# Kernel tuning notes

Hardware: AMD Instinct MI355X
Metric: run time of the kernel (lower is better)

## Reference

```python
import jax, jax.numpy as jnp
import numpy as np

BOUNDS = 1.3
RES = 512
N_COMP = 16
N_LAMB = 3        # n_lamb_params[0]
VEC_PARAM = 3     # vecSize_params[0]
OUT_DIM = 32
N_PTS = 2097152

MAT_X = np.array([0, 0, 1])  # matMode first coord per plane
MAT_Y = np.array([1, 2, 2])  # matMode second coord per plane
VEC_M = np.array([2, 1, 0])  # vecMode


def _sample2d(grid, x, y):
    # grid: [C,H,W]; x,y: [N] in [-1,1]; bilinear, align_corners=True
    C, H, W = grid.shape
    ix = (x + 1.0) * 0.5 * (W - 1)
    iy = (y + 1.0) * 0.5 * (H - 1)
    x0 = jnp.floor(ix)
    y0 = jnp.floor(iy)
    wx = ix - x0
    wy = iy - y0
    x0i = jnp.clip(x0.astype(jnp.int32), 0, W - 1)
    x1i = jnp.clip(x0i + 1, 0, W - 1)
    y0i = jnp.clip(y0.astype(jnp.int32), 0, H - 1)
    y1i = jnp.clip(y0i + 1, 0, H - 1)
    g = lambda yi, xi: grid[:, yi, xi]  # [C,N]
    return (g(y0i, x0i) * (1 - wy) * (1 - wx) + g(y0i, x1i) * (1 - wy) * wx
            + g(y1i, x0i) * wy * (1 - wx) + g(y1i, x1i) * wy * wx)


def _sample1d(vec, y):
    # vec: [C,L]; y: [N] in [-1,1]; linear interp along L (grid width is 1,
    # x coord is always 0 in the torch code so it reduces to 1D)
    C, L = vec.shape
    iy = (y + 1.0) * 0.5 * (L - 1)
    y0 = jnp.floor(iy)
    wy = iy - y0
    y0i = jnp.clip(y0.astype(jnp.int32), 0, L - 1)
    y1i = jnpp_clip = jnp.clip(y0i + 1, 0, L - 1)
    return vec[:, y0i] * (1 - wy) + vec[:, y1i] * wy


def setup_inputs() -> dict:
    key = jax.random.key(0)
    k1, k2, k3, k4, k5 = jax.random.split(key, 5)
    pts = (jax.random.uniform(k1, (N_PTS, 3), jnp.float32) * 2.0 - 1.0) * BOUNDS
    timestamps = jax.random.uniform(k2, (N_PTS, 1), jnp.float32) * 2.0 - 1.0
    scale = 0.1
    planes = scale * jax.random.normal(k3, (3, N_COMP, RES, RES), jnp.float32)
    lines = scale * jax.random.normal(k4, (3, N_COMP, RES), jnp.float32)
    params_grid = scale * jnp.ones((N_LAMB, VEC_PARAM), jnp.float32)
    # torch Linear(19 -> 32, bias=False): weight [out, in]
    W = jax.random.normal(k5, (OUT_DIM, N_COMP + N_LAMB), jnp.float32) * (1.0 / np.sqrt(N_COMP + N_LAMB))
    return {"pts": pts, "timestamps": timestamps, "planes": planes,
            "lines": lines, "params_grid": params_grid, "W": W}


def reference(pts, timestamps, planes, lines, params_grid, W):
    # normalize_aabb with aabb = [[b,b,b],[-b,-b,-b]]
    pts_n = (pts - BOUNDS) * (2.0 / (-2.0 * BOUNDS)) - 1.0  # -> [-1,1]
    # torch code detaches sampling coordinates
    pts_n = jax.lax.stop_gradient(pts_n)
    t = jax.lax.stop_gradient(timestamps[:, 0])
    plane_x = pts_n[:, MAT_X].T  # [3,N]
    plane_y = pts_n[:, MAT_Y].T  # [3,N]
    line_c = pts_n[:, VEC_M].T   # [3,N]
    plane_feat = jax.vmap(_sample2d)(planes, plane_x, plane_y)  # [3,C,N]
    line_feat = jax.vmap(_sample1d)(lines, line_c)              # [3,C,N]
    coef = jnp.sum(plane_feat * line_feat, axis=0)              # [C,N]
    pfeat = _sample1d(params_grid, t)                           # [3,N]
    feats = jnp.concatenate([coef, pfeat], axis=0).T            # [N,19]
    return feats @ W.T                                          # [N,32]
```

## Files before the change

kernel.cpp:

```cpp
#include <hip/hip_runtime.h>
#include <hip/hip_bf16.h>

#define RES 512
#define NC 16
#define NPLANES 3

typedef float f32x4 __attribute__((ext_vector_type(4)));

static __device__ inline float nt_loadf(const float* p) { return __builtin_nontemporal_load(p); }
static __device__ inline void nt_store4(float* p, f32x4 v) {
  __builtin_nontemporal_store(v, (f32x4*)p);
}
static __device__ inline float bf_lo(unsigned u) { return __uint_as_float(u << 16); }
static __device__ inline float bf_hi(unsigned u) { return __uint_as_float(u & 0xFFFF0000u); }

__global__ __launch_bounds__(256) void transpose_planes_k(
    const float* __restrict__ in, __hip_bfloat16* __restrict__ out)
{
  __shared__ float sm[NC][64 + 1];
  int b   = blockIdx.x;
  int xb  = b & 7;
  int y   = (b >> 3) & 511;
  int p   = b >> 12;
  int x0  = xb << 6;
  int tid = threadIdx.x;
#pragma unroll
  for (int k = 0; k < 4; ++k) {
    int e = tid + k * 256;
    int c = e >> 6, x = e & 63;
    sm[c][x] = nt_loadf(&in[(size_t)((p * NC + c) * RES + y) * RES + x0 + x]);
  }
  __syncthreads();
#pragma unroll
  for (int k = 0; k < 4; ++k) {
    int e = tid + k * 256;
    int x = e >> 4, c = e & 15;
    out[(size_t)((p * RES + y) * RES + x0 + x) * NC + c] = __float2bfloat16(sm[c][x]);
  }
}

__global__ void transpose_lines_k(const float* __restrict__ in, float* __restrict__ out)
{
  int i = blockIdx.x * 256 + threadIdx.x;
  if (i >= NPLANES * RES * NC) return;
  int c = i & 15;
  int l = (i >> 4) & 511;
  int p = i >> 13;
  out[i] = nt_loadf(&in[(p * NC + c) * RES + l]);
}

template <bool TP>
__global__ __launch_bounds__(256) void visnerf_main_k(
    const float* __restrict__ pts, const float* __restrict__ ts,
    const __hip_bfloat16* __restrict__ planesb, const float* __restrict__ lines,
    const float* __restrict__ planes_f32, const float* __restrict__ lines_f32,
    const float* __restrict__ pg, const float* __restrict__ W,
    float* __restrict__ out, int N)
{
  __shared__ __align__(16) float sW[32 * 20];
  __shared__ __align__(16) float st[256 * 32];
  __shared__ float spg[9];
  int tid = threadIdx.x;
  for (int e = tid; e < 640; e += 256) {
    int o = e / 20, c = e - o * 20;
    sW[e] = (c < 19) ? W[o * 19 + c] : 0.0f;
  }
  if (tid < 9) spg[tid] = pg[tid];
  __syncthreads();

  int i  = blockIdx.x * 256 + tid;
  int ii = (i < N) ? i : (N - 1);
  float px = nt_loadf(&pts[ii * 3 + 0]);
  float py = nt_loadf(&pts[ii * 3 + 1]);
  float pz = nt_loadf(&pts[ii * 3 + 2]);
  float t  = nt_loadf(&ts[ii]);

  const float kk = (float)(2.0 / (-2.0 * 1.3));
  float nn[3];
  nn[0] = (px - 1.3f) * kk - 1.0f;
  nn[1] = (py - 1.3f) * kk - 1.0f;
  nn[2] = (pz - 1.3f) * kk - 1.0f;

  float feats[20];
#pragma unroll
  for (int c = 0; c < 20; ++c) feats[c] = 0.0f;

  const int matx[3] = {0, 0, 1};
  const int maty[3] = {1, 2, 2};
  const int vecm[3] = {2, 1, 0};

#pragma unroll
  for (int q = 0; q < 3; ++q) {
    float x  = nn[matx[q]], y = nn[maty[q]], lc = nn[vecm[q]];
    float ix = (x + 1.0f) * 0.5f * (float)(RES - 1);
    float iy = (y + 1.0f) * 0.5f * (float)(RES - 1);
    float fx = floorf(ix), fy = floorf(iy);
    float wx = ix - fx, wy = iy - fy;
    int x0 = (int)fx; x0 = x0 < 0 ? 0 : (x0 > RES - 1 ? RES - 1 : x0);
    int y0 = (int)fy; y0 = y0 < 0 ? 0 : (y0 > RES - 1 ? RES - 1 : y0);
    int x1 = (x0 + 1 > RES - 1) ? RES - 1 : x0 + 1;
    int y1 = (y0 + 1 > RES - 1) ? RES - 1 : y0 + 1;

    float il = (lc + 1.0f) * 0.5f * (float)(RES - 1);
    float fl = floorf(il);
    float wl = il - fl;
    int l0 = (int)fl; l0 = l0 < 0 ? 0 : (l0 > RES - 1 ? RES - 1 : l0);
    int l1 = (l0 + 1 > RES - 1) ? RES - 1 : l0 + 1;

    float w00 = (1.0f - wy) * (1.0f - wx);
    float w01 = (1.0f - wy) * wx;
    float w10 = wy * (1.0f - wx);
    float w11 = wy * wx;
    float wl0 = 1.0f - wl;

    if (TP) {
      const uint4* ta = (const uint4*)(planesb + (size_t)((q * RES + y0) * RES + x0) * NC);
      const uint4* tb = (const uint4*)(planesb + (size_t)((q * RES + y0) * RES + x1) * NC);
      const uint4* tc = (const uint4*)(planesb + (size_t)((q * RES + y1) * RES + x0) * NC);
      const uint4* td = (const uint4*)(planesb + (size_t)((q * RES + y1) * RES + x1) * NC);
      const float4* L0 = (const float4*)(lines + (size_t)(q * RES + l0) * NC);
      const float4* L1 = (const float4*)(lines + (size_t)(q * RES + l1) * NC);
#pragma unroll
      for (int h = 0; h < 2; ++h) {
        uint4 ua = ta[h], ub = tb[h], uc = tc[h], ud = td[h];
        float4 e0a = L0[2 * h + 0], e0b = L0[2 * h + 1];
        float4 e1a = L1[2 * h + 0], e1b = L1[2 * h + 1];
        const unsigned* pa = &ua.x;
        const unsigned* pb = &ub.x;
        const unsigned* pc = &uc.x;
        const unsigned* pd = &ud.x;
        const float* q0 = &e0a.x;
        const float* q1 = &e1a.x;
#pragma unroll
        for (int w = 0; w < 4; ++w) {
          int c0 = h * 8 + 2 * w;
          float pf0 = w00 * bf_lo(pa[w]) + w01 * bf_lo(pb[w]) +
                      w10 * bf_lo(pc[w]) + w11 * bf_lo(pd[w]);
          float pf1 = w00 * bf_hi(pa[w]) + w01 * bf_hi(pb[w]) +
                      w10 * bf_hi(pc[w]) + w11 * bf_hi(pd[w]);
          float lf0 = (w < 2) ? (wl0 * q0[2 * w] + wl * q1[2 * w])
                              : (wl0 * (&e0b.x)[2 * w - 4] + wl * (&e1b.x)[2 * w - 4]);
          float lf1 = (w < 2) ? (wl0 * q0[2 * w + 1] + wl * q1[2 * w + 1])
                              : (wl0 * (&e0b.x)[2 * w - 3] + wl * (&e1b.x)[2 * w - 3]);
          feats[c0 + 0] += pf0 * lf0;
          feats[c0 + 1] += pf1 * lf1;
        }
      }
    } else {
#pragma unroll 4
      for (int c = 0; c < NC; ++c) {
        const float* pl = planes_f32 + (size_t)(q * NC + c) * RES * RES;
        float a  = pl[y0 * RES + x0], b = pl[y0 * RES + x1];
        float c2 = pl[y1 * RES + x0], d = pl[y1 * RES + x1];
        const float* ln = lines_f32 + (size_t)(q * NC + c) * RES;
        float lf = ln[l0] * wl0 + ln[l1] * wl;
        feats[c] += (w00 * a + w01 * b + w10 * c2 + w11 * d) * lf;
      }
    }
  }

  {
    float it = (t + 1.0f) * 0.5f * 2.0f;
    float ft = floorf(it);
    float wt = it - ft;
    int t0 = (int)ft; t0 = t0 < 0 ? 0 : (t0 > 2 ? 2 : t0);
    int t1 = (t0 + 1 > 2) ? 2 : t0 + 1;
    feats[16] = spg[0 + t0] * (1.0f - wt) + spg[0 + t1] * wt;
    feats[17] = spg[3 + t0] * (1.0f - wt) + spg[3 + t1] * wt;
    feats[18] = spg[6 + t0] * (1.0f - wt) + spg[6 + t1] * wt;
    feats[19] = 0.0f;
  }

  float res[32];
#pragma unroll
  for (int o = 0; o < 32; ++o) {
    const float4* wr = (const float4*)(sW + o * 20);
    float acc = 0.0f;
#pragma unroll
    for (int k = 0; k < 5; ++k) {
      float4 wv = wr[k];
      acc += feats[4 * k + 0] * wv.x + feats[4 * k + 1] * wv.y +
             feats[4 * k + 2] * wv.z + feats[4 * k + 3] * wv.w;
    }
    res[o] = acc;
  }

#pragma unroll
  for (int o = 0; o < 32; ++o)
    st[tid * 32 + ((o + tid) & 31)] = res[o];
  __syncthreads();

  size_t gbase = (size_t)blockIdx.x * 8192;
  size_t total = (size_t)N * 32;
#pragma unroll
  for (int k = 0; k < 8; ++k) {
    int idx = tid + k * 256;
    int j   = idx * 4;
    int pq  = j >> 5;
    f32x4 v;
    v.x = st[pq * 32 + (((j & 31) + 0 + pq) & 31)];
    v.y = st[pq * 32 + (((j & 31) + 1 + pq) & 31)];
    v.z = st[pq * 32 + (((j & 31) + 2 + pq) & 31)];
    v.w = st[pq * 32 + (((j & 31) + 3 + pq) & 31)];
    if (gbase + j + 4 <= total) {
      nt_store4(out + gbase + j, v);
    }
  }
}

extern "C" void kernel_launch(void* const* d_in, const int* in_sizes, int n_in,
                              void* d_out, int out_size, void* d_ws, size_t ws_size,
                              hipStream_t stream)
{
  const float* pts    = (const float*)d_in[0];
  const float* ts     = (const float*)d_in[1];
  const float* planes = (const float*)d_in[2];
  const float* lines  = (const float*)d_in[3];
  const float* pg     = (const float*)d_in[4];
  const float* W      = (const float*)d_in[5];
  float* out = (float*)d_out;
  int N = in_sizes[0] / 3;

  size_t planesTb_bytes = (size_t)NPLANES * RES * RES * NC * sizeof(__hip_bfloat16);
  size_t linesT_bytes   = (size_t)NPLANES * RES * NC * sizeof(float);
  int blocksMain = (N + 255) / 256;

  if (ws_size >= planesTb_bytes + linesT_bytes) {
    __hip_bfloat16* planesTb = (__hip_bfloat16*)d_ws;
    float* linesT = (float*)((char*)d_ws + planesTb_bytes);
    transpose_planes_k<<<NPLANES * RES * (RES / 64), 256, 0, stream>>>(planes, planesTb);
    transpose_lines_k<<<(NPLANES * RES * NC + 255) / 256, 256, 0, stream>>>(lines, linesT);
    visnerf_main_k<true><<<blocksMain, 256, 0, stream>>>(
        pts, ts, planesTb, linesT, nullptr, nullptr, pg, W, out, N);
  } else {
    visnerf_main_k<false><<<blocksMain, 256, 0, stream>>>(
        pts, ts, nullptr, nullptr, planes, lines, pg, W, out, N);
  }
}
```

Measured before the change: 321.5 us.

## Bin points into spatial cells with counting sort before sampling for gather locality

Adds a counting-sort pipeline (histogram over a 32^3 spatial grid, single-block prefix scan, atomic scatter) that reorders points and timestamps by spatial cell before the main sampling kernel. The sampling kernel then reads points contiguously and writes outputs scattered through the original index, with a block-index swizzle across XCDs. The goal is better cache locality for the random plane and line gathers. In exchange it adds four extra kernel launches, atomics, and an extra pass over the points, and the output stores are now uncoalesced 128-byte rows per thread.

```diff
diff --git a/kernel.cpp b/kernel.cpp
--- a/kernel.cpp
+++ b/kernel.cpp
@@ -4,6 +4,8 @@
 #define RES 512
 #define NC 16
 #define NPLANES 3
+#define NB 32
+#define NCELLS (NB * NB * NB)
 
 typedef float f32x4 __attribute__((ext_vector_type(4)));
 
@@ -13,6 +15,8 @@
 }
 static __device__ inline float bf_lo(unsigned u) { return __uint_as_float(u << 16); }
 static __device__ inline float bf_hi(unsigned u) { return __uint_as_float(u & 0xFFFF0000u); }
+
+#define NORM_K ((float)(2.0 / (-2.0 * 1.3)))
 
 __global__ __launch_bounds__(256) void transpose_planes_k(
     const float* __restrict__ in, __hip_bfloat16* __restrict__ out)
@@ -49,6 +53,197 @@
   out[i] = nt_loadf(&in[(p * NC + c) * RES + l]);
 }
 
+static __device__ inline int cell_of(float px, float py, float pz)
+{
+  float n0 = (px - 1.3f) * NORM_K - 1.0f;
+  float n1 = (py - 1.3f) * NORM_K - 1.0f;
+  float n2 = (pz - 1.3f) * NORM_K - 1.0f;
+  int cx = (int)((n0 + 1.0f) * 16.0f); cx = cx < 0 ? 0 : (cx > NB - 1 ? NB - 1 : cx);
+  int cy = (int)((n1 + 1.0f) * 16.0f); cy = cy < 0 ? 0 : (cy > NB - 1 ? NB - 1 : cy);
+  int cz = (int)((n2 + 1.0f) * 16.0f); cz = cz < 0 ? 0 : (cz > NB - 1 ? NB - 1 : cz);
+  return (cx << 10) | (cy << 5) | cz;
+}
+
+__global__ void zero_hist_k(unsigned* __restrict__ hist)
+{
+  int i = blockIdx.x * 256 + threadIdx.x;
+  if (i < NCELLS) hist[i] = 0;
+}
+
+__global__ void hist_k(const float* __restrict__ pts, unsigned* __restrict__ hist, int N)
+{
+  int i = blockIdx.x * 256 + threadIdx.x;
+  if (i >= N) return;
+  float px = pts[3 * i], py = pts[3 * i + 1], pz = pts[3 * i + 2];
+  atomicAdd(&hist[cell_of(px, py, pz)], 1u);
+}
+
+__global__ __launch_bounds__(256) void prefix_k(
+    const unsigned* __restrict__ hist, unsigned* __restrict__ offs)
+{
+  __shared__ unsigned s[256];
+  int t = threadIdx.x;
+  unsigned sum = 0;
+  for (int k = 0; k < NCELLS / 256; ++k) sum += hist[t * (NCELLS / 256) + k];
+  s[t] = sum;
+  __syncthreads();
+  for (int d = 1; d < 256; d <<= 1) {
+    unsigned v = (t >= d) ? s[t - d] : 0u;
+    __syncthreads();
+    s[t] += v;
+    __syncthreads();
+  }
+  unsigned run = (t == 0) ? 0u : s[t - 1];
+  for (int k = 0; k < NCELLS / 256; ++k) {
+    int c = t * (NCELLS / 256) + k;
+    offs[c] = run;
+    run += hist[c];
+  }
+}
+
+__global__ void scatter_k(const float* __restrict__ pts, const float* __restrict__ ts,
+                          unsigned* __restrict__ offs, f32x4* __restrict__ rec,
+                          unsigned* __restrict__ oidx, int N)
+{
+  int i = blockIdx.x * 256 + threadIdx.x;
+  if (i >= N) return;
+  float px = pts[3 * i], py = pts[3 * i + 1], pz = pts[3 * i + 2];
+  float t  = ts[i];
+  unsigned pos = atomicAdd(&offs[cell_of(px, py, pz)], 1u);
+  f32x4 r; r.x = px; r.y = py; r.z = pz; r.w = t;
+  rec[pos] = r;
+  oidx[pos] = i;
+}
+
+__global__ __launch_bounds__(256) void visnerf_sorted_k(
+    const f32x4* __restrict__ rec, const unsigned* __restrict__ oidx,
+    const __hip_bfloat16* __restrict__ planesb, const float* __restrict__ lines,
+    const float* __restrict__ pg, const float* __restrict__ W,
+    float* __restrict__ out, int N)
+{
+  __shared__ __align__(16) float sW[32 * 20];
+  __shared__ float spg[9];
+  int tid = threadIdx.x;
+  for (int e = tid; e < 640; e += 256) {
+    int o = e / 20, c = e - o * 20;
+    sW[e] = (c < 19) ? W[o * 19 + c] : 0.0f;
+  }
+  if (tid < 9) spg[tid] = pg[tid];
+  __syncthreads();
+
+  int nwg = gridDim.x, bid = blockIdx.x;
+  int sbid = ((nwg & 7) == 0) ? ((bid & 7) * (nwg >> 3) + (bid >> 3)) : bid;
+  int j = sbid * 256 + tid;
+  if (j >= N) return;
+
+  f32x4 r = rec[j];
+  unsigned oi = oidx[j];
+  float t = r.w;
+
+  float nn[3];
+  nn[0] = (r.x - 1.3f) * NORM_K - 1.0f;
+  nn[1] = (r.y - 1.3f) * NORM_K - 1.0f;
+  nn[2] = (r.z - 1.3f) * NORM_K - 1.0f;
+
+  float feats[20];
+#pragma unroll
+  for (int c = 0; c < 20; ++c) feats[c] = 0.0f;
+
+  const int matx[3] = {0, 0, 1};
+  const int maty[3] = {1, 2, 2};
+  const int vecm[3] = {2, 1, 0};
+
+#pragma unroll
+  for (int q = 0; q < 3; ++q) {
+    float x  = nn[matx[q]], y = nn[maty[q]], lc = nn[vecm[q]];
+    float ix = (x + 1.0f) * 0.5f * (float)(RES - 1);
+    float iy = (y + 1.0f) * 0.5f * (float)(RES - 1);
+    float fx = floorf(ix), fy = floorf(iy);
+    float wx = ix - fx, wy = iy - fy;
+    int x0 = (int)fx; x0 = x0 < 0 ? 0 : (x0 > RES - 1 ? RES - 1 : x0);
+    int y0 = (int)fy; y0 = y0 < 0 ? 0 : (y0 > RES - 1 ? RES - 1 : y0);
+    int x1 = (x0 + 1 > RES - 1) ? RES - 1 : x0 + 1;
+    int y1 = (y0 + 1 > RES - 1) ? RES - 1 : y0 + 1;
+
+    float il = (lc + 1.0f) * 0.5f * (float)(RES - 1);
+    float fl = floorf(il);
+    float wl = il - fl;
+    int l0 = (int)fl; l0 = l0 < 0 ? 0 : (l0 > RES - 1 ? RES - 1 : l0);
+    int l1 = (l0 + 1 > RES - 1) ? RES - 1 : l0 + 1;
+
+    float w00 = (1.0f - wy) * (1.0f - wx);
+    float w01 = (1.0f - wy) * wx;
+    float w10 = wy * (1.0f - wx);
+    float w11 = wy * wx;
+    float wl0 = 1.0f - wl;
+
+    const uint4* ta = (const uint4*)(planesb + (size_t)((q * RES + y0) * RES + x0) * NC);
+    const uint4* tb = (const uint4*)(planesb + (size_t)((q * RES + y0) * RES + x1) * NC);
+    const uint4* tc = (const uint4*)(planesb + (size_t)((q * RES + y1) * RES + x0) * NC);
+    const uint4* td = (const uint4*)(planesb + (size_t)((q * RES + y1) * RES + x1) * NC);
+    const float4* L0 = (const float4*)(lines + (size_t)(q * RES + l0) * NC);
+    const float4* L1 = (const float4*)(lines + (size_t)(q * RES + l1) * NC);
+#pragma unroll
+    for (int h = 0; h < 2; ++h) {
+      uint4 ua = ta[h], ub = tb[h], uc = tc[h], ud = td[h];
+      float4 e0a = L0[2 * h + 0], e0b = L0[2 * h + 1];
+      float4 e1a = L1[2 * h + 0], e1b = L1[2 * h + 1];
+      const unsigned* pa = &ua.x;
+      const unsigned* pb = &ub.x;
+      const unsigned* pc = &uc.x;
+      const unsigned* pd = &ud.x;
+      const float* q0 = &e0a.x;
+      const float* q1 = &e1a.x;
+#pragma unroll
+      for (int w = 0; w < 4; ++w) {
+        int c0 = h * 8 + 2 * w;
+        float pf0 = w00 * bf_lo(pa[w]) + w01 * bf_lo(pb[w]) +
+                    w10 * bf_lo(pc[w]) + w11 * bf_lo(pd[w]);
+        float pf1 = w00 * bf_hi(pa[w]) + w01 * bf_hi(pb[w]) +
+                    w10 * bf_hi(pc[w]) + w11 * bf_hi(pd[w]);
+        float lf0 = (w < 2) ? (wl0 * q0[2 * w] + wl * q1[2 * w])
+                            : (wl0 * (&e0b.x)[2 * w - 4] + wl * (&e1b.x)[2 * w - 4]);
+        float lf1 = (w < 2) ? (wl0 * q0[2 * w + 1] + wl * q1[2 * w + 1])
+                            : (wl0 * (&e0b.x)[2 * w - 3] + wl * (&e1b.x)[2 * w - 3]);
+        feats[c0 + 0] += pf0 * lf0;
+        feats[c0 + 1] += pf1 * lf1;
+      }
+    }
+  }
+
+  {
+    float it = (t + 1.0f) * 0.5f * 2.0f;
+    float ft = floorf(it);
+    float wt = it - ft;
+    int t0 = (int)ft; t0 = t0 < 0 ? 0 : (t0 > 2 ? 2 : t0);
+    int t1 = (t0 + 1 > 2) ? 2 : t0 + 1;
+    feats[16] = spg[0 + t0] * (1.0f - wt) + spg[0 + t1] * wt;
+    feats[17] = spg[3 + t0] * (1.0f - wt) + spg[3 + t1] * wt;
+    feats[18] = spg[6 + t0] * (1.0f - wt) + spg[6 + t1] * wt;
+    feats[19] = 0.0f;
+  }
+
+  float* op = out + (size_t)oi * 32;
+#pragma unroll
+  for (int g = 0; g < 8; ++g) {
+    f32x4 v;
+#pragma unroll
+    for (int jj = 0; jj < 4; ++jj) {
+      int o = g * 4 + jj;
+      const float4* wr = (const float4*)(sW + o * 20);
+      float acc = 0.0f;
+#pragma unroll
+      for (int k = 0; k < 5; ++k) {
+        float4 wv = wr[k];
+        acc += feats[4 * k + 0] * wv.x + feats[4 * k + 1] * wv.y +
+               feats[4 * k + 2] * wv.z + feats[4 * k + 3] * wv.w;
+      }
+      v[jj] = acc;
+    }
+    nt_store4(op + 4 * g, v);
+  }
+}
+
 template <bool TP>
 __global__ __launch_bounds__(256) void visnerf_main_k(
     const float* __restrict__ pts, const float* __restrict__ ts,
@@ -75,11 +270,10 @@
   float pz = nt_loadf(&pts[ii * 3 + 2]);
   float t  = nt_loadf(&ts[ii]);
 
-  const float kk = (float)(2.0 / (-2.0 * 1.3));
   float nn[3];
-  nn[0] = (px - 1.3f) * kk - 1.0f;
-  nn[1] = (py - 1.3f) * kk - 1.0f;
-  nn[2] = (pz - 1.3f) * kk - 1.0f;
+  nn[0] = (px - 1.3f) * NORM_K - 1.0f;
+  nn[1] = (py - 1.3f) * NORM_K - 1.0f;
+  nn[2] = (pz - 1.3f) * NORM_K - 1.0f;
 
   float feats[20];
 #pragma unroll
@@ -220,20 +414,43 @@
   const float* W      = (const float*)d_in[5];
   float* out = (float*)d_out;
   int N = in_sizes[0] / 3;
-
-  size_t planesTb_bytes = (size_t)NPLANES * RES * RES * NC * sizeof(__hip_bfloat16);
-  size_t linesT_bytes   = (size_t)NPLANES * RES * NC * sizeof(float);
-  int blocksMain = (N + 255) / 256;
-
-  if (ws_size >= planesTb_bytes + linesT_bytes) {
+  int blocksN = (N + 255) / 256;
+
+  auto align256 = [](size_t x) { return (x + 255) & ~(size_t)255; };
+  size_t planesTb_bytes = align256((size_t)NPLANES * RES * RES * NC * 2);
+  size_t linesT_bytes   = align256((size_t)NPLANES * RES * NC * 4);
+  size_t hist_bytes     = align256((size_t)NCELLS * 4);
+  size_t offs_bytes     = align256((size_t)NCELLS * 4);
+  size_t rec_bytes      = align256((size_t)N * 16);
+  size_t oidx_bytes     = align256((size_t)N * 4);
+  size_t sorted_total = planesTb_bytes + linesT_bytes + hist_bytes + offs_bytes +
+                        rec_bytes + oidx_bytes;
+
+  if (ws_size >= sorted_total) {
+    char* p = (char*)d_ws;
+    __hip_bfloat16* planesTb = (__hip_bfloat16*)p;       p += planesTb_bytes;
+    float*    linesT = (float*)p;                        p += linesT_bytes;
+    unsigned* hist   = (unsigned*)p;                     p += hist_bytes;
+    unsigned* offs   = (unsigned*)p;                     p += offs_bytes;
+    f32x4*    rec    = (f32x4*)p;                        p += rec_bytes;
+    unsigned* oidx   = (unsigned*)p;
+
+    transpose_planes_k<<<NPLANES * RES * (RES / 64), 256, 0, stream>>>(planes, planesTb);
+    transpose_lines_k<<<(NPLANES * RES * NC + 255) / 256, 256, 0, stream>>>(lines, linesT);
+    zero_hist_k<<<(NCELLS + 255) / 256, 256, 0, stream>>>(hist);
+    hist_k<<<blocksN, 256, 0, stream>>>(pts, hist, N);
+    prefix_k<<<1, 256, 0, stream>>>(hist, offs);
+    scatter_k<<<blocksN, 256, 0, stream>>>(pts, ts, offs, rec, oidx, N);
+    visnerf_sorted_k<<<blocksN, 256, 0, stream>>>(rec, oidx, planesTb, linesT, pg, W, out, N);
+  } else if (ws_size >= planesTb_bytes + linesT_bytes) {
     __hip_bfloat16* planesTb = (__hip_bfloat16*)d_ws;
     float* linesT = (float*)((char*)d_ws + planesTb_bytes);
     transpose_planes_k<<<NPLANES * RES * (RES / 64), 256, 0, stream>>>(planes, planesTb);
     transpose_lines_k<<<(NPLANES * RES * NC + 255) / 256, 256, 0, stream>>>(lines, linesT);
-    visnerf_main_k<true><<<blocksMain, 256, 0, stream>>>(
+    visnerf_main_k<true><<<blocksN, 256, 0, stream>>>(
         pts, ts, planesTb, linesT, nullptr, nullptr, pg, W, out, N);
   } else {
-    visnerf_main_k<false><<<blocksMain, 256, 0, stream>>>(
+    visnerf_main_k<false><<<blocksN, 256, 0, stream>>>(
         pts, ts, nullptr, nullptr, planes, lines, pg, W, out, N);
   }
 }
```

Result: slower. 1.135 ms (+253.1%).
